# Kernel tuning notes

Hardware: AMD Instinct MI355X
Metric: run time of the kernel (lower is better)

## Reference

```python
import jax, jax.numpy as jnp
import numpy as np

N = 100000   # nodes
E = 800000   # main-graph edges
EH = 400000  # hull-graph edges
H = 128      # hidden_channels
F = 128      # num_filters
OE = 256     # out_emb_channels
L2 = 256     # int(cha_scale*OE*(1-cha_rate)) = int(2*256*0.5)
OC = 1       # out_channels


def _W(k, i, o):
    return jax.random.normal(k, (i, o), jnp.float32) / np.sqrt(i).astype(np.float32)


def setup_inputs() -> dict:
    key = jax.random.key(0)
    ks = jax.random.split(key, 24)
    return {
        "e2": jax.random.normal(ks[0], (E, H), jnp.float32),
        "i": jax.random.randint(ks[1], (E,), 0, N),
        "fea_hull": jax.random.normal(ks[2], (EH, 16), jnp.float32),
        "edge_index_hull": jax.random.randint(ks[3], (2, EH), 0, N),
        # parameters (stored [in, out])
        "w_hull": _W(ks[4], H, F),                      # lin_hull, no bias
        "w_mlp0": _W(ks[5], 16, F), "b_mlp0": jnp.zeros((F,), jnp.float32),
        "w_mlp1": _W(ks[6], F, F), "b_mlp1": jnp.zeros((F,), jnp.float32),
        "w1_hull": _W(ks[7], F, H), "b1_hull": jnp.zeros((H,), jnp.float32),
        "w2_hull": _W(ks[8], H, L2), "b2_hull": jnp.zeros((L2,), jnp.float32),
        "w_cat": _W(ks[9], L2 + H, H), "b_cat": jnp.zeros((H,), jnp.float32),
        "w_up": _W(ks[10], H, OE), "b_up": jnp.zeros((OE,), jnp.float32),
        "w_l0": _W(ks[11], OE, OE), "b_l0": jnp.zeros((OE,), jnp.float32),
        "w_l1": _W(ks[12], OE, OE), "b_l1": jnp.zeros((OE,), jnp.float32),
        "w_out": _W(ks[13], OE, OC),                    # lin, no bias
    }


def reference(e2, i, fea_hull, edge_index_hull,
              w_hull, w_mlp0, b_mlp0, w_mlp1, b_mlp1,
              w1_hull, b1_hull, w2_hull, b2_hull,
              w_cat, b_cat, w_up, b_up,
              w_l0, b_l0, w_l1, b_l1, w_out):
    act = jax.nn.silu
    # v = scatter_sum(e2, i) over nodes -> [N, H]
    v = jax.ops.segment_sum(e2, i, num_segments=N)
    j_, i_ = edge_index_hull[0], edge_index_hull[1]
    v_hull = v @ w_hull                                        # [N, F]
    W_h = act(fea_hull @ w_mlp0 + b_mlp0) @ w_mlp1 + b_mlp1    # [EH, F]
    e_hull = v_hull[j_] * W_h                                  # gather-multiply
    out_hull = jax.ops.segment_sum(e_hull, i_, num_segments=N) # scatter-sum
    out_hull = act(out_hull @ w1_hull + b1_hull)
    out_hull = out_hull @ w2_hull + b2_hull                    # [N, L2]
    v = act(jnp.concatenate([v, out_hull], axis=1) @ w_cat + b_cat)
    v = v @ w_up + b_up
    v = act(v @ w_l0 + b_l0)
    v = act(v @ w_l1 + b_l1)
    return v @ w_out                                           # [N, OC]
```

## Files before the change

kernel.cpp:

```cpp
#include <hip/hip_runtime.h>
#include <hip/hip_bf16.h>

typedef __bf16 v8bf __attribute__((ext_vector_type(8)));
typedef __bf16 v4bf __attribute__((ext_vector_type(4)));
typedef float  v4f  __attribute__((ext_vector_type(4)));

__device__ __forceinline__ v8bf zero8() {
    v8bf r;
#pragma unroll
    for (int i = 0; i < 8; ++i) r[i] = (__bf16)0.f;
    return r;
}
__device__ __forceinline__ v4f zero4() { v4f r; r[0]=r[1]=r[2]=r[3]=0.f; return r; }

__device__ __forceinline__ v8bf load8bf(const __bf16* p) { return *(const v8bf*)p; }

__device__ __forceinline__ v8bf load8f(const float* p) {
    const float4 x = ((const float4*)p)[0];
    const float4 y = ((const float4*)p)[1];
    v8bf r;
    r[0]=(__bf16)x.x; r[1]=(__bf16)x.y; r[2]=(__bf16)x.z; r[3]=(__bf16)x.w;
    r[4]=(__bf16)y.x; r[5]=(__bf16)y.y; r[6]=(__bf16)y.z; r[7]=(__bf16)y.w;
    return r;
}
__device__ __forceinline__ float silu_f(float x) { return x / (1.f + __expf(-x)); }

struct TDesc { const float* s; __bf16* d; int K; int N; };
struct TPack { TDesc t[9]; };

__global__ __launch_bounds__(256) void transpose_all(TPack p) {
    TDesc td = p.t[blockIdx.x];
    int total = td.K * td.N;
    for (int idx = blockIdx.y * 256 + threadIdx.x; idx < total; idx += 16 * 256) {
        int k = idx / td.N, n = idx - k * td.N;
        td.d[n * td.K + k] = (__bf16)td.s[idx];
    }
}

__global__ __launch_bounds__(256) void hist_both(const int* __restrict__ idxE,
                                                 const int* __restrict__ idxH,
                                                 int* __restrict__ countsE,
                                                 int* __restrict__ countsH,
                                                 int E, int EH) {
    int g = blockIdx.x * 256 + threadIdx.x;
    if (g < E) atomicAdd(&countsE[idxE[g]], 1);
    else if (g < E + EH) atomicAdd(&countsH[idxH[g - E]], 1);
}

__global__ __launch_bounds__(256) void scan_block_sums(const int* __restrict__ counts,
                                                       int* __restrict__ partials,
                                                       int n, int nbS) {
    int t = threadIdx.x, b = blockIdx.x;
    const int* src = counts + ((b >= nbS) ? n : 0);
    int bb = (b >= nbS) ? b - nbS : b;
    int base = bb * 2048 + t * 8;
    int s = 0;
#pragma unroll
    for (int i = 0; i < 8; ++i) {
        int g = base + i;
        s += (g < n) ? src[g] : 0;
    }
#pragma unroll
    for (int off = 32; off; off >>= 1) s += __shfl_down(s, off);
    __shared__ int wsum[4];
    if ((t & 63) == 0) wsum[t >> 6] = s;
    __syncthreads();
    if (t == 0) partials[b] = wsum[0] + wsum[1] + wsum[2] + wsum[3];
}

__global__ void scan_partials_two(int* __restrict__ partials, int nb,
                                  int* __restrict__ row_s, int* __restrict__ row2,
                                  int N, int E, int EH) {
    int w = threadIdx.x >> 6, lane = threadIdx.x & 63;
    if (w > 1) return;
    int* p = partials + w * nb;
    if (nb <= 64) {
        int v = (lane < nb) ? p[lane] : 0;
        int orig = v;
#pragma unroll
        for (int d = 1; d < 64; d <<= 1) {
            int u = __shfl_up(v, d);
            if (lane >= d) v += u;
        }
        if (lane < nb) p[lane] = v - orig;
    } else if (lane == 0) {
        int run = 0;
        for (int i = 0; i < nb; ++i) { int tv = p[i]; p[i] = run; run += tv; }
    }
    if (lane == 0) { if (w == 0) row_s[N] = E; else row2[N] = EH; }
}

__global__ __launch_bounds__(256) void scan_write(const int* __restrict__ counts,
                                                  const int* __restrict__ partials,
                                                  int* __restrict__ row_s,
                                                  int* __restrict__ cursor,
                                                  int* __restrict__ row2,
                                                  int* __restrict__ cursor2,
                                                  int n, int nbS) {
    int t = threadIdx.x, b = blockIdx.x;
    bool hull = b >= nbS;
    const int* src = counts + (hull ? n : 0);
    int bb = hull ? b - nbS : b;
    int* rs = hull ? row2 : row_s;
    int* cu = hull ? cursor2 : cursor;
    int base = bb * 2048 + t * 8;
    int vals[8];
    int tot = 0;
#pragma unroll
    for (int i = 0; i < 8; ++i) {
        int g = base + i;
        vals[i] = (g < n) ? src[g] : 0;
        tot += vals[i];
    }
    __shared__ int sh[256];
    sh[t] = tot;
    __syncthreads();
#pragma unroll
    for (int d = 1; d < 256; d <<= 1) {
        int v = (t >= d) ? sh[t - d] : 0;
        __syncthreads();
        sh[t] += v;
        __syncthreads();
    }
    int run = partials[b] + sh[t] - tot;
#pragma unroll
    for (int i = 0; i < 8; ++i) {
        int g = base + i;
        if (g < n) { rs[g] = run; cu[g] = run; }
        run += vals[i];
    }
}

__global__ __launch_bounds__(256) void rank_scatter_both(const int* __restrict__ idxE,
                                                         const int* __restrict__ idxH,
                                                         int* __restrict__ cursorE,
                                                         int* __restrict__ cursorH,
                                                         int* __restrict__ order,
                                                         int* __restrict__ perm2,
                                                         int* __restrict__ dests2,
                                                         int E, int EH) {
    int g = blockIdx.x * 256 + threadIdx.x;
    if (g < E) {
        int d = idxE[g];
        int pos = atomicAdd(&cursorE[d], 1);
        order[pos] = g;
    } else if (g < E + EH) {
        int e = g - E;
        int d = idxH[e];
        int pos = atomicAdd(&cursorH[d], 1);
        perm2[pos] = e;
        dests2[pos] = d;
    }
}

__global__ __launch_bounds__(256) void gather_v(const float* __restrict__ e2,
                                                const int* __restrict__ order,
                                                const int* __restrict__ row_start,
                                                __bf16* __restrict__ v, int N) {
    __shared__ float4 red[2][4][32];
    int t = threadIdx.x;
    int half = t >> 7, tl = t & 127;
    int grp = tl >> 5, lane = tl & 31;
    int node = blockIdx.x * 2 + half;
    int nc = (node < N) ? node : N - 1;
    int r0 = row_start[nc], r1 = row_start[nc + 1];
    float4 acc = make_float4(0.f, 0.f, 0.f, 0.f);
    int r = r0 + grp;
    for (; r + 4 < r1; r += 8) {
        int e0 = order[r], e1 = order[r + 4];
        float4 a = *(const float4*)(e2 + (size_t)e0 * 128 + lane * 4);
        float4 b = *(const float4*)(e2 + (size_t)e1 * 128 + lane * 4);
        acc.x += a.x + b.x; acc.y += a.y + b.y;
        acc.z += a.z + b.z; acc.w += a.w + b.w;
    }
    if (r < r1) {
        int e0 = order[r];
        float4 a = *(const float4*)(e2 + (size_t)e0 * 128 + lane * 4);
        acc.x += a.x; acc.y += a.y; acc.z += a.z; acc.w += a.w;
    }
    red[half][grp][lane] = acc;
    __syncthreads();
    if (grp == 0 && node < N) {
        float4 s0 = red[half][0][lane], s1 = red[half][1][lane];
        float4 s2 = red[half][2][lane], s3 = red[half][3][lane];
        v4bf o;
        o[0] = (__bf16)(s0.x + s1.x + s2.x + s3.x);
        o[1] = (__bf16)(s0.y + s1.y + s2.y + s3.y);
        o[2] = (__bf16)(s0.z + s1.z + s2.z + s3.z);
        o[3] = (__bf16)(s0.w + s1.w + s2.w + s3.w);
        *(v4bf*)(v + (size_t)node * 128 + lane * 4) = o;
    }
}

__global__ __launch_bounds__(256) void gemm_vhull(const __bf16* __restrict__ v,
                                                  const __bf16* __restrict__ wT,
                                                  __bf16* __restrict__ out, int M) {
    __shared__ __bf16 bS[128 * 136];
    int t = threadIdx.x, wave = t >> 6, lane = t & 63, q = lane >> 4, l16 = lane & 15;
    int m0 = blockIdx.x * 128;
    {
        int row = t >> 1, half = t & 1;
        const v8bf* g = (const v8bf*)(wT + (size_t)row * 128 + half * 64);
        v8bf* d = (v8bf*)(bS + row * 136 + half * 64);
#pragma unroll
        for (int i = 0; i < 8; ++i) d[i] = g[i];
    }
    __syncthreads();
    int r0 = m0 + wave * 32;
    v4f acc[2][8];
#pragma unroll
    for (int i = 0; i < 2; ++i)
#pragma unroll
        for (int j = 0; j < 8; ++j) acc[i][j] = zero4();
    int ar0 = r0 + l16;      if (ar0 >= M) ar0 = M - 1;
    int ar1 = r0 + 16 + l16; if (ar1 >= M) ar1 = M - 1;
#pragma unroll
    for (int kt = 0; kt < 4; ++kt) {
        v8bf a0 = load8bf(v + (size_t)ar0 * 128 + kt * 32 + q * 8);
        v8bf a1 = load8bf(v + (size_t)ar1 * 128 + kt * 32 + q * 8);
#pragma unroll
        for (int nt = 0; nt < 8; ++nt) {
            v8bf b = *(const v8bf*)(bS + (nt * 16 + l16) * 136 + kt * 32 + q * 8);
            acc[0][nt] = __builtin_amdgcn_mfma_f32_16x16x32_bf16(a0, b, acc[0][nt], 0, 0, 0);
            acc[1][nt] = __builtin_amdgcn_mfma_f32_16x16x32_bf16(a1, b, acc[1][nt], 0, 0, 0);
        }
    }
#pragma unroll
    for (int tile = 0; tile < 2; ++tile)
#pragma unroll
        for (int nt = 0; nt < 8; ++nt)
#pragma unroll
            for (int r = 0; r < 4; ++r) {
                int row = r0 + tile * 16 + q * 4 + r;
                if (row < M) out[(size_t)row * 128 + nt * 16 + l16] = (__bf16)acc[tile][nt][r];
            }
}

__global__ __launch_bounds__(256) void hull_msg(const float* __restrict__ fea,
                                                const int* __restrict__ perm,
                                                const int* __restrict__ jidx,
                                                const int* __restrict__ dests,
                                                const __bf16* __restrict__ w0T,
                                                const float* __restrict__ bias0,
                                                const __bf16* __restrict__ w1T,
                                                const float* __restrict__ bias1,
                                                const __bf16* __restrict__ vhull,
                                                float* __restrict__ oh32, int EH) {
    __shared__ __bf16 hb[64][136];
    __shared__ __bf16 whS[64][136];
    __shared__ int jb[64];
    __shared__ int db[64];
    int t = threadIdx.x;
    int wave = t >> 6, lane = t & 63, q = lane >> 4, l16 = lane & 15;
    int r0 = blockIdx.x * 64;
    if (t < 64) {
        int slot = r0 + t;
        int sc = (slot < EH) ? slot : EH - 1;
        jb[t] = jidx[perm[sc]];
        db[t] = (slot < EH) ? dests[slot] : -1;
    }
    {
        int slot = r0 + wave * 16 + l16; if (slot >= EH) slot = EH - 1;
        int e = perm[slot];
        v8bf a = (q < 2) ? load8f(fea + (size_t)e * 16 + q * 8) : zero8();
        v4f acc[8];
#pragma unroll
        for (int i = 0; i < 8; ++i) acc[i] = zero4();
#pragma unroll
        for (int nt = 0; nt < 8; ++nt) {
            v8bf b = (q < 2) ? load8bf(w0T + (size_t)(nt * 16 + l16) * 16 + q * 8) : zero8();
            acc[nt] = __builtin_amdgcn_mfma_f32_16x16x32_bf16(a, b, acc[nt], 0, 0, 0);
        }
#pragma unroll
        for (int nt = 0; nt < 8; ++nt) {
            int col = nt * 16 + l16;
            float bc = bias0[col];
#pragma unroll
            for (int r = 0; r < 4; ++r) {
                int rowL = wave * 16 + q * 4 + r;
                hb[rowL][col] = (__bf16)silu_f(acc[nt][r] + bc);
            }
        }
    }
    __syncthreads();
    {
        v8bf af[4];
#pragma unroll
        for (int kt = 0; kt < 4; ++kt)
            af[kt] = *(const v8bf*)&hb[wave * 16 + l16][kt * 32 + q * 8];
        v4f acc[8];
#pragma unroll
        for (int i = 0; i < 8; ++i) acc[i] = zero4();
#pragma unroll
        for (int kt = 0; kt < 4; ++kt)
#pragma unroll
            for (int nt = 0; nt < 8; ++nt) {
                v8bf b = load8bf(w1T + (size_t)(nt * 16 + l16) * 128 + kt * 32 + q * 8);
                acc[nt] = __builtin_amdgcn_mfma_f32_16x16x32_bf16(af[kt], b, acc[nt], 0, 0, 0);
            }
#pragma unroll
        for (int nt = 0; nt < 8; ++nt) {
            int col = nt * 16 + l16;
            float bc = bias1[col];
#pragma unroll
            for (int r = 0; r < 4; ++r) {
                int rowL = wave * 16 + q * 4 + r;
                whS[rowL][col] = (__bf16)(acc[nt][r] + bc);
            }
        }
    }
    __syncthreads();
    {
        int row = t >> 2, sub = t & 3;
        int slot = r0 + row;
        if (slot < EH) {
            int j = jb[row];
            const v8bf* vr = (const v8bf*)(vhull + (size_t)j * 128 + sub * 32);
#pragma unroll
            for (int i = 0; i < 4; ++i) {
                v8bf wv = *(const v8bf*)&whS[row][sub * 32 + i * 8];
                v8bf vv = vr[i];
                v8bf o;
#pragma unroll
                for (int k = 0; k < 8; ++k) o[k] = (__bf16)((float)wv[k] * (float)vv[k]);
                *(v8bf*)&whS[row][sub * 32 + i * 8] = o;
            }
        }
    }
    __syncthreads();
    {
        int c = t & 127, half = t >> 7;
        int rbeg = half * 32, rend = rbeg + 32;
        float run = 0.f; int cur = -1;
        for (int r = rbeg; r < rend; ++r) {
            int d = db[r];
            if (d != cur) {
                if (cur >= 0) atomicAdd(oh32 + (size_t)cur * 128 + c, run);
                run = 0.f; cur = d;
            }
            if (cur >= 0) run += (float)whS[r][c];
        }
        if (cur >= 0) atomicAdd(oh32 + (size_t)cur * 128 + c, run);
    }
}

#define ALD 392
#define BLD 392

template<int K, int NCH, bool SILU>
__device__ __forceinline__ void gemm_stage(const __bf16* __restrict__ wT,
                                           const float* __restrict__ bias,
                                           __bf16* actS, __bf16* bS,
                                           int srcCol, int dstCol,
                                           int wave, int lane, int t) {
    int q = lane >> 4, l16 = lane & 15;
    v4f acc[NCH * 4];
#pragma unroll
    for (int j = 0; j < NCH * 4; ++j) acc[j] = zero4();

    int brow = t >> 3, sub = t & 7;
    constexpr int RV = K / 64;
    v8bf breg[RV];
    {
        const v8bf* g = (const v8bf*)(wT + (size_t)brow * K) + sub * RV;
#pragma unroll
        for (int i = 0; i < RV; ++i) breg[i] = g[i];
    }
#pragma unroll
    for (int c = 0; c < NCH; ++c) {
        __syncthreads();
        {
            v8bf* d = (v8bf*)(bS + brow * BLD) + sub * RV;
#pragma unroll
            for (int i = 0; i < RV; ++i) d[i] = breg[i];
        }
        if (c + 1 < NCH) {
            const v8bf* g = (const v8bf*)(wT + (size_t)((c + 1) * 64 + brow) * K) + sub * RV;
#pragma unroll
            for (int i = 0; i < RV; ++i) breg[i] = g[i];
        }
        asm volatile("s_waitcnt lgkmcnt(0)" ::: "memory");
        __builtin_amdgcn_s_barrier();
        __builtin_amdgcn_sched_barrier(0);
#pragma unroll
        for (int kt = 0; kt < K / 32; ++kt) {
            v8bf a0 = *(const v8bf*)(actS + (wave * 16 + l16) * ALD + srcCol + kt * 32 + q * 8);
#pragma unroll
            for (int nt = 0; nt < 4; ++nt) {
                v8bf b = *(const v8bf*)(bS + (nt * 16 + l16) * BLD + kt * 32 + q * 8);
                acc[c * 4 + nt] = __builtin_amdgcn_mfma_f32_16x16x32_bf16(a0, b, acc[c * 4 + nt], 0, 0, 0);
            }
        }
    }
#pragma unroll
    for (int j = 0; j < NCH * 4; ++j) {
        float bc = bias[j * 16 + l16];
#pragma unroll
        for (int r = 0; r < 4; ++r) {
            int row = wave * 16 + q * 4 + r;
            float val = acc[j][r] + bc;
            if (SILU) val = silu_f(val);
            actS[row * ALD + dstCol + j * 16 + l16] = (__bf16)val;
        }
    }
}

__global__ __launch_bounds__(512, 1) void node_chain(
    const __bf16* __restrict__ v, const float* __restrict__ oh,
    const __bf16* __restrict__ w1T, const float* __restrict__ b1,
    const __bf16* __restrict__ w2T, const float* __restrict__ b2,
    const __bf16* __restrict__ wcatT, const float* __restrict__ bcat,
    const __bf16* __restrict__ wupT, const float* __restrict__ bup,
    const __bf16* __restrict__ wl0T, const float* __restrict__ bl0,
    const __bf16* __restrict__ wl1T, const float* __restrict__ bl1,
    const float* __restrict__ wout, float* __restrict__ out, int M) {
    __shared__ __bf16 actS[128 * ALD];
    __shared__ __bf16 bS[64 * BLD];
    int t = threadIdx.x, wave = t >> 6, lane = t & 63;
    int m0b = blockIdx.x * 128;

    {
        int row = wave * 16 + (lane >> 2), quarter = lane & 3;
        int gr = m0b + row; if (gr >= M) gr = M - 1;
        const v8bf* sv = (const v8bf*)(v + (size_t)gr * 128 + quarter * 32);
        const float* so = oh + (size_t)gr * 128 + quarter * 32;
        v8bf* dv = (v8bf*)(actS + row * ALD + quarter * 32);
        v8bf* doh = (v8bf*)(actS + row * ALD + 256 + quarter * 32);
#pragma unroll
        for (int i = 0; i < 4; ++i) { dv[i] = sv[i]; doh[i] = load8f(so + i * 8); }
    }

    gemm_stage<128, 2, true >(w1T,   b1,   actS, bS, 256, 128, wave, lane, t);
    gemm_stage<128, 4, false>(w2T,   b2,   actS, bS, 128, 128, wave, lane, t);
    gemm_stage<384, 2, true >(wcatT, bcat, actS, bS, 0,   0,   wave, lane, t);
    gemm_stage<128, 4, false>(wupT,  bup,  actS, bS, 0,   128, wave, lane, t);
    gemm_stage<256, 4, true >(wl0T,  bl0,  actS, bS, 128, 128, wave, lane, t);
    gemm_stage<256, 4, true >(wl1T,  bl1,  actS, bS, 128, 128, wave, lane, t);

    {
        int row = wave * 16 + (lane >> 2), quarter = lane & 3;
        const __bf16* ap = actS + row * ALD + 128 + quarter * 64;
        const float* wq = wout + quarter * 64;
        float s = 0.f;
#pragma unroll
        for (int c8 = 0; c8 < 8; ++c8) {
            v8bf a8 = *(const v8bf*)(ap + c8 * 8);
            const float4 w0 = ((const float4*)(wq + c8 * 8))[0];
            const float4 w1 = ((const float4*)(wq + c8 * 8))[1];
            s += (float)a8[0] * w0.x + (float)a8[1] * w0.y + (float)a8[2] * w0.z + (float)a8[3] * w0.w;
            s += (float)a8[4] * w1.x + (float)a8[5] * w1.y + (float)a8[6] * w1.z + (float)a8[7] * w1.w;
        }
        s += __shfl_xor(s, 1);
        s += __shfl_xor(s, 2);
        int gr = m0b + row;
        if (quarter == 0 && gr < M) out[gr] = s;
    }
}

static inline char* align16(char* p) {
    return (char*)(((uintptr_t)p + 15) & ~(uintptr_t)15);
}

extern "C" void kernel_launch(void* const* d_in, const int* in_sizes, int n_in,
                              void* d_out, int out_size, void* d_ws, size_t ws_size,
                              hipStream_t stream) {
    const float* e2      = (const float*)d_in[0];
    const int*   iidx    = (const int*)d_in[1];
    const float* fea     = (const float*)d_in[2];
    const int*   eih     = (const int*)d_in[3];
    const float* w_hull  = (const float*)d_in[4];
    const float* w_mlp0  = (const float*)d_in[5];
    const float* b_mlp0  = (const float*)d_in[6];
    const float* w_mlp1  = (const float*)d_in[7];
    const float* b_mlp1  = (const float*)d_in[8];
    const float* w1_hull = (const float*)d_in[9];
    const float* b1_hull = (const float*)d_in[10];
    const float* w2_hull = (const float*)d_in[11];
    const float* b2_hull = (const float*)d_in[12];
    const float* w_cat   = (const float*)d_in[13];
    const float* b_cat   = (const float*)d_in[14];
    const float* w_up    = (const float*)d_in[15];
    const float* b_up    = (const float*)d_in[16];
    const float* w_l0    = (const float*)d_in[17];
    const float* b_l0    = (const float*)d_in[18];
    const float* w_l1    = (const float*)d_in[19];
    const float* b_l1    = (const float*)d_in[20];
    const float* w_out   = (const float*)d_in[21];

    int N  = out_size;
    int E  = in_sizes[0] / 128;
    int EH = in_sizes[2] / 16;
    const int* jidx_h = eih;
    const int* iidx_h = eih + EH;

    char* p = (char*)d_ws;
    __bf16* v     = (__bf16*)p; p += (size_t)N * 128 * 2;
    __bf16* vhull = (__bf16*)p; p += (size_t)N * 128 * 2;
    float*  oh32  = (float*)p;  p += (size_t)N * 128 * 4;
    __bf16* wp = (__bf16*)p;
    __bf16* w_hullT = wp; wp += 128 * 128;
    __bf16* w0T     = wp; wp += 128 * 16;
    __bf16* w1mT    = wp; wp += 128 * 128;
    __bf16* w1hT    = wp; wp += 128 * 128;
    __bf16* w2hT    = wp; wp += 256 * 128;
    __bf16* wcatT   = wp; wp += 128 * 384;
    __bf16* wupT    = wp; wp += 256 * 128;
    __bf16* wl0T    = wp; wp += 256 * 256;
    __bf16* wl1T    = wp; wp += 256 * 256;
    p = align16((char*)wp);
    int* counts   = (int*)p; p += (size_t)N * 4 * 2;
    int* row_s    = (int*)p; p += (size_t)(N + 1) * 4;
    int* cursor   = (int*)p; p += (size_t)N * 4;
    int* row2     = (int*)p; p += (size_t)(N + 1) * 4;
    int* cursor2  = (int*)p; p += (size_t)N * 4;
    int* order    = (int*)p; p += (size_t)E * 4;
    int* perm2    = (int*)p; p += (size_t)EH * 4;
    int* dests2   = (int*)p; p += (size_t)EH * 4;
    int* partials = (int*)p; p += 512 * 4;
    int* counts2  = counts + N;

    TPack tp;
    tp.t[0] = { w_hull,  w_hullT, 128, 128 };
    tp.t[1] = { w_mlp0,  w0T,      16, 128 };
    tp.t[2] = { w_mlp1,  w1mT,    128, 128 };
    tp.t[3] = { w1_hull, w1hT,    128, 128 };
    tp.t[4] = { w2_hull, w2hT,    128, 256 };
    tp.t[5] = { w_cat,   wcatT,   384, 128 };
    tp.t[6] = { w_up,    wupT,    128, 256 };
    tp.t[7] = { w_l0,    wl0T,    256, 256 };
    tp.t[8] = { w_l1,    wl1T,    256, 256 };
    transpose_all<<<dim3(9, 16), 256, 0, stream>>>(tp);

    (void)hipMemsetAsync(counts, 0, (size_t)N * 4 * 2, stream);
    (void)hipMemsetAsync(oh32, 0, (size_t)N * 128 * 4, stream);

    const int nbS = (N + 2047) / 2048;

    hist_both<<<(E + EH + 255) / 256, 256, 0, stream>>>(iidx, iidx_h, counts, counts2, E, EH);
    scan_block_sums<<<2 * nbS, 256, 0, stream>>>(counts, partials, N, nbS);
    scan_partials_two<<<1, 128, 0, stream>>>(partials, nbS, row_s, row2, N, E, EH);
    scan_write<<<2 * nbS, 256, 0, stream>>>(counts, partials, row_s, cursor, row2, cursor2, N, nbS);
    rank_scatter_both<<<(E + EH + 255) / 256, 256, 0, stream>>>(iidx, iidx_h, cursor, cursor2,
                                                                order, perm2, dests2, E, EH);

    gather_v<<<(N + 1) / 2, 256, 0, stream>>>(e2, order, row_s, v, N);

    gemm_vhull<<<(N + 127) / 128, 256, 0, stream>>>(v, w_hullT, vhull, N);

    hull_msg<<<(EH + 63) / 64, 256, 0, stream>>>(fea, perm2, jidx_h, dests2, w0T, b_mlp0,
                                                 w1mT, b_mlp1, vhull, oh32, EH);

    node_chain<<<(N + 127) / 128, 512, 0, stream>>>(v, oh32, w1hT, b1_hull, w2hT, b2_hull,
                                                    wcatT, b_cat, wupT, b_up,
                                                    wl0T, b_l0, wl1T, b_l1,
                                                    w_out, (float*)d_out, N);
}
```

Baseline: 1.117 ms.

## Partition hull messages by destination node and accumulate in shared memory

Each hull_msg block now owns 16 destination nodes and walks their CSR-sorted edge range using row2 offsets. Per-node sums are accumulated in a shared fp32 buffer and written once as bf16, replacing the global fp32 atomicAdd scatter. This also drops the memset of the fp32 output buffer and halves what node_chain reads. In exchange, per-block work now depends on node degree, which can unbalance blocks. The code also assumes N is a multiple of 16, since row2[n0+16] and the output stores have no bounds check.

```diff
diff --git a/kernel.cpp b/kernel.cpp
--- a/kernel.cpp
+++ b/kernel.cpp
@@ -240,107 +240,124 @@
                                                 const int* __restrict__ perm,
                                                 const int* __restrict__ jidx,
                                                 const int* __restrict__ dests,
+                                                const int* __restrict__ row2,
                                                 const __bf16* __restrict__ w0T,
                                                 const float* __restrict__ bias0,
                                                 const __bf16* __restrict__ w1T,
                                                 const float* __restrict__ bias1,
                                                 const __bf16* __restrict__ vhull,
-                                                float* __restrict__ oh32, int EH) {
+                                                __bf16* __restrict__ oh, int N) {
     __shared__ __bf16 hb[64][136];
     __shared__ __bf16 whS[64][136];
+    __shared__ float nodeAcc[2][16][128];
     __shared__ int jb[64];
     __shared__ int db[64];
     int t = threadIdx.x;
     int wave = t >> 6, lane = t & 63, q = lane >> 4, l16 = lane & 15;
-    int r0 = blockIdx.x * 64;
-    if (t < 64) {
-        int slot = r0 + t;
-        int sc = (slot < EH) ? slot : EH - 1;
-        jb[t] = jidx[perm[sc]];
-        db[t] = (slot < EH) ? dests[slot] : -1;
-    }
+    int n0 = blockIdx.x * 16;
+    int r0 = row2[n0], rend = row2[n0 + 16];
+
     {
-        int slot = r0 + wave * 16 + l16; if (slot >= EH) slot = EH - 1;
-        int e = perm[slot];
-        v8bf a = (q < 2) ? load8f(fea + (size_t)e * 16 + q * 8) : zero8();
-        v4f acc[8];
-#pragma unroll
-        for (int i = 0; i < 8; ++i) acc[i] = zero4();
-#pragma unroll
-        for (int nt = 0; nt < 8; ++nt) {
-            v8bf b = (q < 2) ? load8bf(w0T + (size_t)(nt * 16 + l16) * 16 + q * 8) : zero8();
-            acc[nt] = __builtin_amdgcn_mfma_f32_16x16x32_bf16(a, b, acc[nt], 0, 0, 0);
-        }
-#pragma unroll
-        for (int nt = 0; nt < 8; ++nt) {
-            int col = nt * 16 + l16;
-            float bc = bias0[col];
-#pragma unroll
-            for (int r = 0; r < 4; ++r) {
-                int rowL = wave * 16 + q * 4 + r;
-                hb[rowL][col] = (__bf16)silu_f(acc[nt][r] + bc);
-            }
-        }
+        float* z = &nodeAcc[0][0][0];
+#pragma unroll
+        for (int i = 0; i < 16; ++i) z[t + i * 256] = 0.f;
     }
     __syncthreads();
+
+    for (int tr0 = r0; tr0 < rend; tr0 += 64) {
+        if (t < 64) {
+            int slot = tr0 + t;
+            int sc = (slot < rend) ? slot : rend - 1;
+            jb[t] = jidx[perm[sc]];
+            db[t] = dests[sc];
+        }
+        bool active = (tr0 + wave * 16) < rend;
+        if (active) {
+            int slot = tr0 + wave * 16 + l16; if (slot >= rend) slot = rend - 1;
+            int e = perm[slot];
+            v8bf a = (q < 2) ? load8f(fea + (size_t)e * 16 + q * 8) : zero8();
+            v4f acc[8];
+#pragma unroll
+            for (int i = 0; i < 8; ++i) acc[i] = zero4();
+#pragma unroll
+            for (int nt = 0; nt < 8; ++nt) {
+                v8bf b = (q < 2) ? load8bf(w0T + (size_t)(nt * 16 + l16) * 16 + q * 8) : zero8();
+                acc[nt] = __builtin_amdgcn_mfma_f32_16x16x32_bf16(a, b, acc[nt], 0, 0, 0);
+            }
+#pragma unroll
+            for (int nt = 0; nt < 8; ++nt) {
+                int col = nt * 16 + l16;
+                float bc = bias0[col];
+#pragma unroll
+                for (int r = 0; r < 4; ++r) {
+                    int rowL = wave * 16 + q * 4 + r;
+                    hb[rowL][col] = (__bf16)silu_f(acc[nt][r] + bc);
+                }
+            }
+            v8bf af[4];
+#pragma unroll
+            for (int kt = 0; kt < 4; ++kt)
+                af[kt] = *(const v8bf*)&hb[wave * 16 + l16][kt * 32 + q * 8];
+            v4f acc2[8];
+#pragma unroll
+            for (int i = 0; i < 8; ++i) acc2[i] = zero4();
+#pragma unroll
+            for (int kt = 0; kt < 4; ++kt)
+#pragma unroll
+                for (int nt = 0; nt < 8; ++nt) {
+                    v8bf b = load8bf(w1T + (size_t)(nt * 16 + l16) * 128 + kt * 32 + q * 8);
+                    acc2[nt] = __builtin_amdgcn_mfma_f32_16x16x32_bf16(af[kt], b, acc2[nt], 0, 0, 0);
+                }
+#pragma unroll
+            for (int nt = 0; nt < 8; ++nt) {
+                int col = nt * 16 + l16;
+                float bc = bias1[col];
+#pragma unroll
+                for (int r = 0; r < 4; ++r) {
+                    int rowL = wave * 16 + q * 4 + r;
+                    whS[rowL][col] = (__bf16)(acc2[nt][r] + bc);
+                }
+            }
+        }
+        __syncthreads();
+        {
+            int row = t >> 2, sub = t & 3;
+            int slot = tr0 + row;
+            if (slot < rend) {
+                int j = jb[row];
+                const v8bf* vr = (const v8bf*)(vhull + (size_t)j * 128 + sub * 32);
+#pragma unroll
+                for (int i = 0; i < 4; ++i) {
+                    v8bf wv = *(const v8bf*)&whS[row][sub * 32 + i * 8];
+                    v8bf vv = vr[i];
+                    v8bf o;
+#pragma unroll
+                    for (int k = 0; k < 8; ++k) o[k] = (__bf16)((float)wv[k] * (float)vv[k]);
+                    *(v8bf*)&whS[row][sub * 32 + i * 8] = o;
+                }
+            }
+        }
+        __syncthreads();
+        {
+            int half = t >> 7, c = t & 127;
+            int rb = half * 32;
+#pragma unroll 4
+            for (int r = rb; r < rb + 32; ++r) {
+                int slot = tr0 + r;
+                if (slot < rend)
+                    nodeAcc[half][db[r] - n0][c] += (float)whS[r][c];
+            }
+        }
+        __syncthreads();
+    }
+
     {
-        v8bf af[4];
-#pragma unroll
-        for (int kt = 0; kt < 4; ++kt)
-            af[kt] = *(const v8bf*)&hb[wave * 16 + l16][kt * 32 + q * 8];
-        v4f acc[8];
-#pragma unroll
-        for (int i = 0; i < 8; ++i) acc[i] = zero4();
-#pragma unroll
-        for (int kt = 0; kt < 4; ++kt)
-#pragma unroll
-            for (int nt = 0; nt < 8; ++nt) {
-                v8bf b = load8bf(w1T + (size_t)(nt * 16 + l16) * 128 + kt * 32 + q * 8);
-                acc[nt] = __builtin_amdgcn_mfma_f32_16x16x32_bf16(af[kt], b, acc[nt], 0, 0, 0);
-            }
-#pragma unroll
-        for (int nt = 0; nt < 8; ++nt) {
-            int col = nt * 16 + l16;
-            float bc = bias1[col];
-#pragma unroll
-            for (int r = 0; r < 4; ++r) {
-                int rowL = wave * 16 + q * 4 + r;
-                whS[rowL][col] = (__bf16)(acc[nt][r] + bc);
-            }
-        }
-    }
-    __syncthreads();
-    {
-        int row = t >> 2, sub = t & 3;
-        int slot = r0 + row;
-        if (slot < EH) {
-            int j = jb[row];
-            const v8bf* vr = (const v8bf*)(vhull + (size_t)j * 128 + sub * 32);
-#pragma unroll
-            for (int i = 0; i < 4; ++i) {
-                v8bf wv = *(const v8bf*)&whS[row][sub * 32 + i * 8];
-                v8bf vv = vr[i];
-                v8bf o;
-#pragma unroll
-                for (int k = 0; k < 8; ++k) o[k] = (__bf16)((float)wv[k] * (float)vv[k]);
-                *(v8bf*)&whS[row][sub * 32 + i * 8] = o;
-            }
-        }
-    }
-    __syncthreads();
-    {
-        int c = t & 127, half = t >> 7;
-        int rbeg = half * 32, rend = rbeg + 32;
-        float run = 0.f; int cur = -1;
-        for (int r = rbeg; r < rend; ++r) {
-            int d = db[r];
-            if (d != cur) {
-                if (cur >= 0) atomicAdd(oh32 + (size_t)cur * 128 + c, run);
-                run = 0.f; cur = d;
-            }
-            if (cur >= 0) run += (float)whS[r][c];
-        }
-        if (cur >= 0) atomicAdd(oh32 + (size_t)cur * 128 + c, run);
+        int node = t >> 4, c0 = (t & 15) * 8;
+        v8bf o;
+#pragma unroll
+        for (int i = 0; i < 8; ++i)
+            o[i] = (__bf16)(nodeAcc[0][node][c0 + i] + nodeAcc[1][node][c0 + i]);
+        *(v8bf*)(oh + (size_t)(n0 + node) * 128 + c0) = o;
     }
 }
 
@@ -406,7 +423,7 @@
 }
 
 __global__ __launch_bounds__(512, 1) void node_chain(
-    const __bf16* __restrict__ v, const float* __restrict__ oh,
+    const __bf16* __restrict__ v, const __bf16* __restrict__ oh,
     const __bf16* __restrict__ w1T, const float* __restrict__ b1,
     const __bf16* __restrict__ w2T, const float* __restrict__ b2,
     const __bf16* __restrict__ wcatT, const float* __restrict__ bcat,
@@ -423,11 +440,11 @@
         int row = wave * 16 + (lane >> 2), quarter = lane & 3;
         int gr = m0b + row; if (gr >= M) gr = M - 1;
         const v8bf* sv = (const v8bf*)(v + (size_t)gr * 128 + quarter * 32);
-        const float* so = oh + (size_t)gr * 128 + quarter * 32;
+        const v8bf* so = (const v8bf*)(oh + (size_t)gr * 128 + quarter * 32);
         v8bf* dv = (v8bf*)(actS + row * ALD + quarter * 32);
         v8bf* doh = (v8bf*)(actS + row * ALD + 256 + quarter * 32);
 #pragma unroll
-        for (int i = 0; i < 4; ++i) { dv[i] = sv[i]; doh[i] = load8f(so + i * 8); }
+        for (int i = 0; i < 4; ++i) { dv[i] = sv[i]; doh[i] = so[i]; }
     }
 
     gemm_stage<128, 2, true >(w1T,   b1,   actS, bS, 256, 128, wave, lane, t);
@@ -496,7 +513,7 @@
     char* p = (char*)d_ws;
     __bf16* v     = (__bf16*)p; p += (size_t)N * 128 * 2;
     __bf16* vhull = (__bf16*)p; p += (size_t)N * 128 * 2;
-    float*  oh32  = (float*)p;  p += (size_t)N * 128 * 4;
+    __bf16* oh    = (__bf16*)p; p += (size_t)N * 128 * 2;
     __bf16* wp = (__bf16*)p;
     __bf16* w_hullT = wp; wp += 128 * 128;
     __bf16* w0T     = wp; wp += 128 * 16;
@@ -532,7 +549,6 @@
     transpose_all<<<dim3(9, 16), 256, 0, stream>>>(tp);
 
     (void)hipMemsetAsync(counts, 0, (size_t)N * 4 * 2, stream);
-    (void)hipMemsetAsync(oh32, 0, (size_t)N * 128 * 4, stream);
 
     const int nbS = (N + 2047) / 2048;
 
@@ -547,10 +563,10 @@
 
     gemm_vhull<<<(N + 127) / 128, 256, 0, stream>>>(v, w_hullT, vhull, N);
 
-    hull_msg<<<(EH + 63) / 64, 256, 0, stream>>>(fea, perm2, jidx_h, dests2, w0T, b_mlp0,
-                                                 w1mT, b_mlp1, vhull, oh32, EH);
-
-    node_chain<<<(N + 127) / 128, 512, 0, stream>>>(v, oh32, w1hT, b1_hull, w2hT, b2_hull,
+    hull_msg<<<(N + 15) / 16, 256, 0, stream>>>(fea, perm2, jidx_h, dests2, row2,
+                                                w0T, b_mlp0, w1mT, b_mlp1, vhull, oh, N);
+
+    node_chain<<<(N + 127) / 128, 512, 0, stream>>>(v, oh, w1hT, b1_hull, w2hT, b2_hull,
                                                     wcatT, b_cat, wupT, b_up,
                                                     wl0T, b_l0, wl1T, b_l1,
                                                     w_out, (float*)d_out, N);
```

After: 1.200 ms. 1.07x slower.
